# Kernel optimization log

Hardware: AMD Instinct MI355X
Metric: run time of the kernel (lower is better)

Reference implementation:

```python
import jax, jax.numpy as jnp
import numpy as np

B, S, H, NH = 4, 2048, 1024, 16
HS = H // NH  # head size 64


def setup_inputs() -> dict:
    key = jax.random.key(0)
    ks = jax.random.split(key, 12)
    inv = 1.0 / np.sqrt(H)
    d = {
        "query": jax.random.normal(ks[0], (B, S, H), jnp.float32),
        "key": jax.random.normal(ks[1], (B, S, H), jnp.float32),
        "value": jax.random.normal(ks[2], (B, S, H), jnp.float32),
        "causal_mask": jnp.tril(jnp.ones((S, S), dtype=bool)),
        "Wq": jax.random.uniform(ks[3], (H, H), jnp.float32, -inv, inv),
        "bq": jax.random.uniform(ks[4], (H,), jnp.float32, -inv, inv),
        "Wk": jax.random.uniform(ks[5], (H, H), jnp.float32, -inv, inv),
        "bk": jax.random.uniform(ks[6], (H,), jnp.float32, -inv, inv),
        "Wv": jax.random.uniform(ks[7], (H, H), jnp.float32, -inv, inv),
        "bv": jax.random.uniform(ks[8], (H,), jnp.float32, -inv, inv),
        "Wo": jax.random.uniform(ks[9], (H, H), jnp.float32, -inv, inv),
        "bo": jax.random.uniform(ks[10], (H,), jnp.float32, -inv, inv),
    }
    return d


def reference(query, key, value, causal_mask, Wq, bq, Wk, bk, Wv, bv, Wo, bo):
    # Linear projections (torch Linear: x @ W.T + b)
    q = query @ Wq.T + bq
    k = key @ Wk.T + bk
    v = value @ Wv.T + bv
    # [B, NH, S, HS]
    q = q.reshape(B, S, NH, HS).transpose(0, 2, 1, 3)
    k = k.reshape(B, S, NH, HS).transpose(0, 2, 1, 3)
    v = v.reshape(B, S, NH, HS).transpose(0, 2, 1, 3)
    scores = jnp.einsum("bhqd,bhkd->bhqk", q, k) / jnp.sqrt(jnp.float32(HS))
    scores = jnp.where(causal_mask[None, None, :, :], scores, -jnp.inf)
    attn = jax.nn.softmax(scores, axis=-1)
    ctx = jnp.einsum("bhqk,bhkd->bhqd", attn, v)
    ctx = ctx.transpose(0, 2, 1, 3).reshape(B, S, H)
    return ctx @ Wo.T + bo
```

## Files before the change

kernel.cpp:

```cpp
#include <hip/hip_runtime.h>
#include <hip/hip_bf16.h>
#include <math.h>

#define B_  4
#define S_  2048
#define H_  1024
#define NH_ 16
#define HS_ 64

typedef __attribute__((ext_vector_type(8))) short bf16x8;
typedef __attribute__((ext_vector_type(4))) short s16x4;
typedef __attribute__((ext_vector_type(4))) float f32x4;
typedef __attribute__((ext_vector_type(4))) unsigned u32x4;

#define QSCALE_ (0.125f * 1.44269504f)

__device__ __forceinline__ short f2bf(float f) {
    unsigned u = __builtin_bit_cast(unsigned, f);
    u += 0x7FFFu + ((u >> 16) & 1u);
    return (short)(u >> 16);
}

typedef __attribute__((address_space(3))) void lds_void;
typedef const __attribute__((address_space(1))) void g_void;
__device__ __forceinline__ void gl_lds16(const void* g, void* l) {
    __builtin_amdgcn_global_load_lds((g_void*)g, (lds_void*)l, 16, 0, 0);
}


__global__ __launch_bounds__(256) void cvt_all_k(
    const float* __restrict__ a0, const float* __restrict__ a1,
    const float* __restrict__ a2, const float* __restrict__ w0,
    const float* __restrict__ w1, const float* __restrict__ w2,
    const float* __restrict__ w3,
    short* o0, short* o1, short* o2, short* o3, short* o4, short* o5, short* o6)
{
    const int y = blockIdx.y;
    const float* ins[7]  = {a0, a1, a2, w0, w1, w2, w3};
    short*       outs[7] = {o0, o1, o2, o3, o4, o5, o6};
    const int n8 = (y < 3) ? (int)((size_t)B_ * S_ * H_ / 8) : (int)((size_t)H_ * H_ / 8);
    const int i = blockIdx.x * 256 + threadIdx.x;
    if (i >= n8) return;
    const float4* p = (const float4*)ins[y] + (size_t)i * 2;
    float4 a = p[0], b = p[1];
    bf16x8 o;
    o[0] = f2bf(a.x); o[1] = f2bf(a.y); o[2] = f2bf(a.z); o[3] = f2bf(a.w);
    o[4] = f2bf(b.x); o[5] = f2bf(b.y); o[6] = f2bf(b.z); o[7] = f2bf(b.w);
    *(bf16x8*)(outs[y] + (size_t)i * 8) = o;
}

__device__ __forceinline__ void gemm_core(
    const short* __restrict__ A, const short* __restrict__ W,
    int m0, int n0, short* As, short* Ws, f32x4 acc[4][4])
{
    const int tid  = threadIdx.x;
    const int w    = tid >> 6;
    const int lane = tid & 63;
    const int l15  = lane & 15;
    const int q4   = lane >> 4;
    const int wm   = w >> 1;
    const int wn   = w & 1;
    const int K    = 1024;
    const int swz  = l15 & 7;

    const char* Abase = (const char*)A + (size_t)m0 * K * 2;
    const char* Wbase = (const char*)W + (size_t)n0 * K * 2;

    #pragma unroll
    for (int mi = 0; mi < 4; ++mi)
        #pragma unroll
        for (int ni = 0; ni < 4; ++ni)
            acc[mi][ni] = (f32x4){0.f, 0.f, 0.f, 0.f};

    for (int k0 = 0; k0 < K; k0 += 64) {
        __syncthreads();
        #pragma unroll
        for (int t = 0; t < 4; ++t) {
            const int ob  = t * 4096 + w * 1024;
            const int idx = t * 256 + w * 64 + lane;
            const int row = idx >> 3;
            const int sc  = (idx & 7) ^ (row & 7);
            gl_lds16(Abase + (size_t)row * (K * 2) + k0 * 2 + sc * 16, (char*)As + ob);
            gl_lds16(Wbase + (size_t)row * (K * 2) + k0 * 2 + sc * 16, (char*)Ws + ob);
        }
        __syncthreads();

        #pragma unroll
        for (int kh = 0; kh < 2; ++kh) {
            bf16x8 af[4], bf[4];
            #pragma unroll
            for (int mi = 0; mi < 4; ++mi)
                af[mi] = *(const bf16x8*)(As + (wm * 64 + mi * 16 + l15) * 64
                                             + (((kh * 4 + q4) ^ swz) * 8));
            #pragma unroll
            for (int ni = 0; ni < 4; ++ni)
                bf[ni] = *(const bf16x8*)(Ws + (wn * 64 + ni * 16 + l15) * 64
                                             + (((kh * 4 + q4) ^ swz) * 8));
            #pragma unroll
            for (int mi = 0; mi < 4; ++mi)
                #pragma unroll
                for (int ni = 0; ni < 4; ++ni)
                    acc[mi][ni] = __builtin_amdgcn_mfma_f32_16x16x32_bf16(
                        af[mi], bf[ni], acc[mi][ni], 0, 0, 0);
        }
    }
}

__global__ __launch_bounds__(256) void gemm_proj_k(
    const short* __restrict__ Aq, const short* __restrict__ Wqb,
    const float* __restrict__ bq, short* __restrict__ qb,
    const short* __restrict__ Ak, const short* __restrict__ Wkb,
    const float* __restrict__ bk, short* __restrict__ kb,
    const short* __restrict__ Wvb, const short* __restrict__ Av,
    const float* __restrict__ bv, short* __restrict__ vtb)
{
    __shared__ short As[128 * 64];
    __shared__ short Ws[128 * 64];

    const int z = blockIdx.z;
    const short *A, *W; const float* bias; short* out;
    if (z == 0)      { A = Aq;  W = Wqb; bias = bq; out = qb;  }
    else if (z == 1) { A = Ak;  W = Wkb; bias = bk; out = kb;  }
    else             { A = Wvb; W = Av;  bias = bv; out = vtb; }
    const int m0 = (z == 2 ? blockIdx.y : blockIdx.x) * 128;
    const int n0 = (z == 2 ? blockIdx.x : blockIdx.y) * 128;

    f32x4 acc[4][4];
    gemm_core(A, W, m0, n0, As, Ws, acc);

    const int tid  = threadIdx.x;
    const int w    = tid >> 6;
    const int lane = tid & 63;
    const int l15  = lane & 15;
    const int q4   = lane >> 4;
    const int wm   = w >> 1;
    const int wn   = w & 1;

    #pragma unroll
    for (int mi = 0; mi < 4; ++mi) {
        #pragma unroll
        for (int r = 0; r < 4; ++r) {
            const int m = m0 + wm * 64 + mi * 16 + q4 * 4 + r;
            #pragma unroll
            for (int ni = 0; ni < 4; ++ni) {
                const int n = n0 + wn * 64 + ni * 16 + l15;
                float v = acc[mi][ni][r] + bias[z == 2 ? m : n];
                if (z == 0) v *= QSCALE_;
                if (z != 2) {
                    const int b = m >> 11, s = m & (S_ - 1);
                    const int h = n >> 6,  d = n & (HS_ - 1);
                    out[(((size_t)b * NH_ + h) * S_ + s) * HS_ + d] = f2bf(v);
                } else {
                    const int b = n >> 11, s = n & (S_ - 1);
                    const int h = m >> 6,  d = m & (HS_ - 1);
                    out[(((size_t)b * NH_ + h) * HS_ + d) * S_ + s] = f2bf(v);
                }
            }
        }
    }
}

__global__ __launch_bounds__(256) void gemm_out_k(
    const short* __restrict__ A, const short* __restrict__ W,
    const float* __restrict__ bias, float* __restrict__ Cout)
{
    __shared__ short As[128 * 64];
    __shared__ short Ws[128 * 64];
    const int m0 = blockIdx.x * 128;
    const int n0 = blockIdx.y * 128;

    f32x4 acc[4][4];
    gemm_core(A, W, m0, n0, As, Ws, acc);

    const int tid  = threadIdx.x;
    const int w    = tid >> 6;
    const int lane = tid & 63;
    const int l15  = lane & 15;
    const int q4   = lane >> 4;
    const int wm   = w >> 1;
    const int wn   = w & 1;

    #pragma unroll
    for (int mi = 0; mi < 4; ++mi)
        #pragma unroll
        for (int r = 0; r < 4; ++r) {
            const int m = m0 + wm * 64 + mi * 16 + q4 * 4 + r;
            #pragma unroll
            for (int ni = 0; ni < 4; ++ni) {
                const int n = n0 + wn * 64 + ni * 16 + l15;
                Cout[(size_t)m * H_ + n] = acc[mi][ni][r] + bias[n];
            }
        }
}

__global__ __launch_bounds__(256) void attn_mfma(
    const short* __restrict__ Q, const short* __restrict__ K,
    const short* __restrict__ VT, short* __restrict__ O)
{
    __shared__ short Ks[2][64 * 64];
    __shared__ short Vt[2][64 * 64];

    const int tid  = threadIdx.x;
    const int w    = tid >> 6;
    const int lane = tid & 63;
    const int l15  = lane & 15;
    const int q4   = lane >> 4;
    const int swz  = l15 & 7;
    const int bh   = blockIdx.y;
    const size_t base = (size_t)bh * S_ * HS_;
    const int b = bh >> 4;
    const int h = bh & 15;

#define STAGE_KV(slot_, kt_)                                                      \
    do {                                                                          \
        _Pragma("unroll")                                                         \
        for (int t = 0; t < 2; ++t) {                                             \
            const int ob  = (slot_) * 8192 + t * 4096 + w * 1024;                 \
            const int idx = t * 256 + w * 64 + lane;        \
            const int r   = idx >> 3;                                             \
            const int sc  = (idx & 7) ^ (r & 7);          \
            gl_lds16(K + base + (size_t)((kt_) * 64 + r) * HS_ + sc * 8,          \
                     (char*)Ks + ob);                                             \
            gl_lds16(VT + base + (size_t)r * S_ + (kt_) * 64 + sc * 8,            \
                     (char*)Vt + ob);                                             \
        }                                                                         \
    } while (0)

    #pragma unroll 1
    for (int pass = 0; pass < 2; ++pass) {
        const int qt = pass ? (15 - blockIdx.x) : blockIdx.x;
        const int ktmax = 2 * qt + 1;

        STAGE_KV(0, 0);

        bf16x8 aQ[2][2];
        #pragma unroll
        for (int mi = 0; mi < 2; ++mi) {
            const int qrow = qt * 128 + w * 32 + mi * 16 + l15;
            #pragma unroll
            for (int kh = 0; kh < 2; ++kh)
                aQ[mi][kh] = *(const bf16x8*)(Q + base + (size_t)qrow * HS_ + kh * 32 + q4 * 8);
        }

        f32x4 accO[2][4];
        float lsum[2];
        #pragma unroll
        for (int mi = 0; mi < 2; ++mi) {
            #pragma unroll
            for (int db = 0; db < 4; ++db) accO[mi][db] = (f32x4){0.f, 0.f, 0.f, 0.f};
            lsum[mi] = 0.f;
        }

        __syncthreads();

        for (int kt = 0; kt <= ktmax; ++kt) {
            const int cur = kt & 1;
            if (kt < ktmax) STAGE_KV(cur ^ 1, kt + 1);

            f32x4 sT[2][4];
            const short* KsBase = &Ks[cur][0];
            __builtin_amdgcn_s_setprio(1);
            #pragma unroll
            for (int nb = 0; nb < 4; ++nb) {
                const short* krow = KsBase + (nb * 16 + l15) * 64;
                bf16x8 k0 = *(const bf16x8*)(krow + ((q4 ^ swz) * 8));
                bf16x8 k1 = *(const bf16x8*)(krow + (((4 + q4) ^ swz) * 8));
                #pragma unroll
                for (int mi = 0; mi < 2; ++mi) {
                    f32x4 a = (f32x4){0.f, 0.f, 0.f, 0.f};
                    a = __builtin_amdgcn_mfma_f32_16x16x32_bf16(k0, aQ[mi][0], a, 0, 0, 0);
                    a = __builtin_amdgcn_mfma_f32_16x16x32_bf16(k1, aQ[mi][1], a, 0, 0, 0);
                    sT[mi][nb] = a;
                }
            }
            __builtin_amdgcn_s_setprio(0);

            if (kt >= 2 * qt) {
                #pragma unroll
                for (int mi = 0; mi < 2; ++mi) {
                    const int qrow = qt * 128 + w * 32 + mi * 16 + l15;
                    #pragma unroll
                    for (int nb = 0; nb < 4; ++nb)
                        #pragma unroll
                        for (int r = 0; r < 4; ++r) {
                            const int kj = kt * 64 + nb * 16 + q4 * 4 + r;
                            if (kj > qrow) sT[mi][nb][r] = -INFINITY;
                        }
                }
            }

            bf16x8 aP[2][2];
            #pragma unroll
            for (int mi = 0; mi < 2; ++mi) {
                float p[4][4];
                #pragma unroll
                for (int nb = 0; nb < 4; ++nb)
                    #pragma unroll
                    for (int r = 0; r < 4; ++r) {
                        float pv;
                        asm("v_exp_f32 %0, %1" : "=v"(pv) : "v"(sT[mi][nb][r]));
                        lsum[mi] += pv;
                        p[nb][r] = pv;
                    }
                #pragma unroll
                for (int hf = 0; hf < 2; ++hf) {
                    unsigned w0, w1, w2, w3;
                    asm("v_cvt_pk_bf16_f32 %0, %1, %2" : "=v"(w0) : "v"(p[2*hf][0]),   "v"(p[2*hf][1]));
                    asm("v_cvt_pk_bf16_f32 %0, %1, %2" : "=v"(w1) : "v"(p[2*hf][2]),   "v"(p[2*hf][3]));
                    asm("v_cvt_pk_bf16_f32 %0, %1, %2" : "=v"(w2) : "v"(p[2*hf+1][0]), "v"(p[2*hf+1][1]));
                    asm("v_cvt_pk_bf16_f32 %0, %1, %2" : "=v"(w3) : "v"(p[2*hf+1][2]), "v"(p[2*hf+1][3]));
                    u32x4 pw; pw[0] = w0; pw[1] = w1; pw[2] = w2; pw[3] = w3;
                    aP[mi][hf] = __builtin_bit_cast(bf16x8, pw);
                }
            }

            const short* VtBase = &Vt[cur][0];
            __builtin_amdgcn_s_setprio(1);
            #pragma unroll
            for (int db = 0; db < 4; ++db) {
                const short* vrow = VtBase + (db * 16 + l15) * 64;
                #pragma unroll
                for (int hf = 0; hf < 2; ++hf) {
                    const int lc0 = 4 * hf + (q4 >> 1);
                    const int lc1 = lc0 + 2;
                    s16x4 vlo = *(const s16x4*)(vrow + ((lc0 ^ swz) * 8) + 4 * (q4 & 1));
                    s16x4 vhi = *(const s16x4*)(vrow + ((lc1 ^ swz) * 8) + 4 * (q4 & 1));
                    bf16x8 vf = __builtin_shufflevector(vlo, vhi, 0, 1, 2, 3, 4, 5, 6, 7);
                    #pragma unroll
                    for (int mi = 0; mi < 2; ++mi)
                        accO[mi][db] = __builtin_amdgcn_mfma_f32_16x16x32_bf16(
                            aP[mi][hf], vf, accO[mi][db], 0, 0, 0);
                }
            }
            __builtin_amdgcn_s_setprio(0);

            __syncthreads();
        }

        #pragma unroll
        for (int mi = 0; mi < 2; ++mi) {
            float ls = lsum[mi];
            ls += __shfl_xor(ls, 16);
            ls += __shfl_xor(ls, 32);
            #pragma unroll
            for (int r = 0; r < 4; ++r) {
                const float inv = 1.f / __shfl(ls, q4 * 4 + r);
                const int orow = qt * 128 + w * 32 + mi * 16 + q4 * 4 + r;
                short* op = O + ((size_t)(b * S_ + orow)) * H_ + h * HS_;
                #pragma unroll
                for (int db = 0; db < 4; ++db)
                    op[db * 16 + l15] = f2bf(accO[mi][db][r] * inv);
            }
        }
    }
#undef STAGE_KV
}

extern "C" void kernel_launch(void* const* d_in, const int* in_sizes, int n_in,
                              void* d_out, int out_size, void* d_ws, size_t ws_size,
                              hipStream_t stream)
{
    const float* query = (const float*)d_in[0];
    const float* key   = (const float*)d_in[1];
    const float* value = (const float*)d_in[2];
    const float* Wq = (const float*)d_in[4];
    const float* bq = (const float*)d_in[5];
    const float* Wk = (const float*)d_in[6];
    const float* bk = (const float*)d_in[7];
    const float* Wv = (const float*)d_in[8];
    const float* bv = (const float*)d_in[9];
    const float* Wo = (const float*)d_in[10];
    const float* bo = (const float*)d_in[11];
    float* out = (float*)d_out;

    const size_t EA = (size_t)B_ * S_ * H_;
    const size_t EW = (size_t)H_ * H_;

    short* Aq  = (short*)d_ws;
    short* Ak  = Aq  + EA;
    short* Av  = Ak  + EA;
    short* Wqb = Av  + EA;
    short* Wkb = Wqb + EW;
    short* Wvb = Wkb + EW;
    short* Wob = Wvb + EW;
    short* qb  = Wob + EW;
    short* kb  = qb  + EA;
    short* vtb = kb  + EA;
    short* cb  = vtb + EA;

    const int M = B_ * S_;

    cvt_all_k<<<dim3((int)(EA / 8 / 256), 7), 256, 0, stream>>>(
        query, key, value, Wq, Wk, Wv, Wo,
        Aq, Ak, Av, Wqb, Wkb, Wvb, Wob);

    gemm_proj_k<<<dim3(M / 128, H_ / 128, 3), 256, 0, stream>>>(
        Aq, Wqb, bq, qb, Ak, Wkb, bk, kb, Wvb, Av, bv, vtb);

    attn_mfma<<<dim3(S_ / 256, B_ * NH_), 256, 0, stream>>>(qb, kb, vtb, cb);

    gemm_out_k<<<dim3(M / 128, H_ / 128), 256, 0, stream>>>(cb, Wob, bo, out);
}
```

Measured before the change: 349.7 us.

## Swap GEMM operand roles for vectorized epilogue stores and remap attention block order

Q/K projection and output GEMMs now compute the transposed product (weights as the M operand), so each lane's four accumulator rows map to contiguous head-dim columns. That lets the epilogue add a float4 bias and emit packed bf16x4 or float4 stores instead of scalar ones. The V projection path keeps scalar stores with a hoisted bias load. The attention kernel also remaps the flat block index so consecutive blocks cover different batch-heads, aiming for better balance and cache locality, at the cost of changed memory access patterns and inline asm conversion.

```diff
diff --git a/kernel.cpp b/kernel.cpp
--- a/kernel.cpp
+++ b/kernel.cpp
@@ -118,15 +118,15 @@
     __shared__ short Ws[128 * 64];
 
     const int z = blockIdx.z;
-    const short *A, *W; const float* bias; short* out;
-    if (z == 0)      { A = Aq;  W = Wqb; bias = bq; out = qb;  }
-    else if (z == 1) { A = Ak;  W = Wkb; bias = bk; out = kb;  }
-    else             { A = Wvb; W = Av;  bias = bv; out = vtb; }
-    const int m0 = (z == 2 ? blockIdx.y : blockIdx.x) * 128;
-    const int n0 = (z == 2 ? blockIdx.x : blockIdx.y) * 128;
+    const short *Wm, *Am; const float* bias; short* out;
+    if (z == 0)      { Wm = Wqb; Am = Aq; bias = bq; out = qb;  }
+    else if (z == 1) { Wm = Wkb; Am = Ak; bias = bk; out = kb;  }
+    else             { Wm = Wvb; Am = Av; bias = bv; out = vtb; }
+    const int m0 = blockIdx.y * 128;
+    const int n0 = blockIdx.x * 128;
 
     f32x4 acc[4][4];
-    gemm_core(A, W, m0, n0, As, Ws, acc);
+    gemm_core(Wm, Am, m0, n0, As, Ws, acc);
 
     const int tid  = threadIdx.x;
     const int w    = tid >> 6;
@@ -136,24 +136,43 @@
     const int wm   = w >> 1;
     const int wn   = w & 1;
 
-    #pragma unroll
-    for (int mi = 0; mi < 4; ++mi) {
-        #pragma unroll
-        for (int r = 0; r < 4; ++r) {
-            const int m = m0 + wm * 64 + mi * 16 + q4 * 4 + r;
+    if (z != 2) {
+        #pragma unroll
+        for (int mi = 0; mi < 4; ++mi) {
+            const int nbase = m0 + wm * 64 + mi * 16 + q4 * 4;
+            const float4 b4 = *(const float4*)(bias + nbase);
+            const int d0 = nbase & 63;
+            const int h  = nbase >> 6;
             #pragma unroll
             for (int ni = 0; ni < 4; ++ni) {
-                const int n = n0 + wn * 64 + ni * 16 + l15;
-                float v = acc[mi][ni][r] + bias[z == 2 ? m : n];
-                if (z == 0) v *= QSCALE_;
-                if (z != 2) {
-                    const int b = m >> 11, s = m & (S_ - 1);
-                    const int h = n >> 6,  d = n & (HS_ - 1);
-                    out[(((size_t)b * NH_ + h) * S_ + s) * HS_ + d] = f2bf(v);
-                } else {
-                    const int b = n >> 11, s = n & (S_ - 1);
-                    const int h = m >> 6,  d = m & (HS_ - 1);
-                    out[(((size_t)b * NH_ + h) * HS_ + d) * S_ + s] = f2bf(v);
+                const int m = n0 + wn * 64 + ni * 16 + l15;
+                const int bb = m >> 11, s = m & (S_ - 1);
+                float v0 = acc[mi][ni][0] + b4.x;
+                float v1 = acc[mi][ni][1] + b4.y;
+                float v2 = acc[mi][ni][2] + b4.z;
+                float v3 = acc[mi][ni][3] + b4.w;
+                if (z == 0) { v0 *= QSCALE_; v1 *= QSCALE_; v2 *= QSCALE_; v3 *= QSCALE_; }
+                unsigned lo, hi;
+                asm("v_cvt_pk_bf16_f32 %0, %1, %2" : "=v"(lo) : "v"(v0), "v"(v1));
+                asm("v_cvt_pk_bf16_f32 %0, %1, %2" : "=v"(hi) : "v"(v2), "v"(v3));
+                uint2 pk; pk.x = lo; pk.y = hi;
+                *(uint2*)(out + (((size_t)bb * NH_ + h) * S_ + s) * HS_ + d0) = pk;
+            }
+        }
+    } else {
+        #pragma unroll
+        for (int mi = 0; mi < 4; ++mi) {
+            #pragma unroll
+            for (int r = 0; r < 4; ++r) {
+                const int m = m0 + wm * 64 + mi * 16 + q4 * 4 + r;
+                const float bm = bias[m];
+                const int h = m >> 6, d = m & (HS_ - 1);
+                #pragma unroll
+                for (int ni = 0; ni < 4; ++ni) {
+                    const int n = n0 + wn * 64 + ni * 16 + l15;
+                    const int bb = n >> 11, s = n & (S_ - 1);
+                    out[(((size_t)bb * NH_ + h) * HS_ + d) * S_ + s] =
+                        f2bf(acc[mi][ni][r] + bm);
                 }
             }
         }
@@ -161,16 +180,16 @@
 }
 
 __global__ __launch_bounds__(256) void gemm_out_k(
-    const short* __restrict__ A, const short* __restrict__ W,
+    const short* __restrict__ Wo, const short* __restrict__ Cb,
     const float* __restrict__ bias, float* __restrict__ Cout)
 {
     __shared__ short As[128 * 64];
     __shared__ short Ws[128 * 64];
-    const int m0 = blockIdx.x * 128;
-    const int n0 = blockIdx.y * 128;
+    const int m0 = blockIdx.y * 128;
+    const int n0 = blockIdx.x * 128;
 
     f32x4 acc[4][4];
-    gemm_core(A, W, m0, n0, As, Ws, acc);
+    gemm_core(Wo, Cb, m0, n0, As, Ws, acc);
 
     const int tid  = threadIdx.x;
     const int w    = tid >> 6;
@@ -181,16 +200,20 @@
     const int wn   = w & 1;
 
     #pragma unroll
-    for (int mi = 0; mi < 4; ++mi)
-        #pragma unroll
-        for (int r = 0; r < 4; ++r) {
-            const int m = m0 + wm * 64 + mi * 16 + q4 * 4 + r;
-            #pragma unroll
-            for (int ni = 0; ni < 4; ++ni) {
-                const int n = n0 + wn * 64 + ni * 16 + l15;
-                Cout[(size_t)m * H_ + n] = acc[mi][ni][r] + bias[n];
-            }
-        }
+    for (int mi = 0; mi < 4; ++mi) {
+        const int nbase = m0 + wm * 64 + mi * 16 + q4 * 4;
+        const float4 b4 = *(const float4*)(bias + nbase);
+        #pragma unroll
+        for (int ni = 0; ni < 4; ++ni) {
+            const int m = n0 + wn * 64 + ni * 16 + l15;
+            float4 vv;
+            vv.x = acc[mi][ni][0] + b4.x;
+            vv.y = acc[mi][ni][1] + b4.y;
+            vv.z = acc[mi][ni][2] + b4.z;
+            vv.w = acc[mi][ni][3] + b4.w;
+            *(float4*)(Cout + (size_t)m * H_ + nbase) = vv;
+        }
+    }
 }
 
 __global__ __launch_bounds__(256) void attn_mfma(
@@ -206,7 +229,11 @@
     const int l15  = lane & 15;
     const int q4   = lane >> 4;
     const int swz  = l15 & 7;
-    const int bh   = blockIdx.y;
+
+    const int f   = blockIdx.y * 8 + blockIdx.x;
+    const int bh  = (f & 7) * 8 + ((f >> 3) & 7);
+    const int qx  = f >> 6;
+
     const size_t base = (size_t)bh * S_ * HS_;
     const int b = bh >> 4;
     const int h = bh & 15;
@@ -228,7 +255,7 @@
 
     #pragma unroll 1
     for (int pass = 0; pass < 2; ++pass) {
-        const int qt = pass ? (15 - blockIdx.x) : blockIdx.x;
+        const int qt = pass ? (15 - qx) : qx;
         const int ktmax = 2 * qt + 1;
 
         STAGE_KV(0, 0);
@@ -399,5 +426,5 @@
 
     attn_mfma<<<dim3(S_ / 256, B_ * NH_), 256, 0, stream>>>(qb, kb, vtb, cb);
 
-    gemm_out_k<<<dim3(M / 128, H_ / 128), 256, 0, stream>>>(cb, Wob, bo, out);
-}
+    gemm_out_k<<<dim3(M / 128, H_ / 128), 256, 0, stream>>>(Wob, cb, bo, out);
+}
```

New measurement: 318.1 us. -9.1%, faster.
